# Kernel tuning notes

Measured on AMD Instinct MI355X. Metric: run time of the kernel, lower is better.

The kernel has to match this reference:

```python
import jax, jax.numpy as jnp
import numpy as np

LN2 = float(np.log(2.0))

def ssp(x):
    # ShiftedSoftplus: softplus(x) - log(2)
    return jax.nn.softplus(x) - LN2

N_NODES = 40000
N_EDGES = 640000
HIDDEN = 128
N_FILTERS = 128
N_GAUSS = 50
CUTOFF = 10.0

def setup_inputs() -> dict:
    key = jax.random.key(0)
    ks = jax.random.split(key, 12)
    s = 0.05
    x = jax.random.normal(ks[0], (N_NODES, HIDDEN), dtype=jnp.float32)
    edge_index = jax.random.randint(ks[1], (2, N_EDGES), 0, N_NODES)
    edge_weight = jax.random.uniform(ks[2], (N_EDGES,), dtype=jnp.float32) * CUTOFF
    edge_attr = jax.random.normal(ks[3], (N_EDGES, N_GAUSS), dtype=jnp.float32)
    # filter MLP params (Linear(num_gaussians,num_filters), ssp, Linear(num_filters,num_filters))
    mlp_w1 = jax.random.normal(ks[4], (N_FILTERS, N_GAUSS), dtype=jnp.float32) * s
    mlp_b1 = jnp.zeros((N_FILTERS,), dtype=jnp.float32)
    mlp_w2 = jax.random.normal(ks[5], (N_FILTERS, N_FILTERS), dtype=jnp.float32) * s
    mlp_b2 = jnp.zeros((N_FILTERS,), dtype=jnp.float32)
    # CFConv linears: lin1 (no bias), lin2 (bias)
    lin1_w = jax.random.normal(ks[6], (N_FILTERS, HIDDEN), dtype=jnp.float32) * s
    lin2_w = jax.random.normal(ks[7], (HIDDEN, N_FILTERS), dtype=jnp.float32) * s
    lin2_b = jnp.zeros((HIDDEN,), dtype=jnp.float32)
    # output linear
    lin_w = jax.random.normal(ks[8], (HIDDEN, HIDDEN), dtype=jnp.float32) * s
    lin_b = jnp.zeros((HIDDEN,), dtype=jnp.float32)
    return {
        "x": x, "edge_index": edge_index, "edge_weight": edge_weight, "edge_attr": edge_attr,
        "mlp_w1": mlp_w1, "mlp_b1": mlp_b1, "mlp_w2": mlp_w2, "mlp_b2": mlp_b2,
        "lin1_w": lin1_w, "lin2_w": lin2_w, "lin2_b": lin2_b,
        "lin_w": lin_w, "lin_b": lin_b,
    }

def reference(x, edge_index, edge_weight, edge_attr,
              mlp_w1, mlp_b1, mlp_w2, mlp_b2,
              lin1_w, lin2_w, lin2_b, lin_w, lin_b):
    src, dst = edge_index[0], edge_index[1]
    # cosine envelope
    C = 0.5 * (jnp.cos(edge_weight * jnp.pi / CUTOFF) + 1.0)  # (E,)
    # filter MLP on Gaussian-smeared distances
    W = ssp(edge_attr @ mlp_w1.T + mlp_b1) @ mlp_w2.T + mlp_b2  # (E, F)
    W = W * C[:, None]
    # CFConv: lin1 -> gather x_j -> multiply -> scatter-add -> lin2
    h = x @ lin1_w.T                                            # (N, F)
    msg = h[src] * W                                            # (E, F)
    agg = jax.ops.segment_sum(msg, dst, num_segments=x.shape[0])  # (N, F)
    h2 = agg @ lin2_w.T + lin2_b                                # (N, H)
    # activation + output projection
    out = ssp(h2) @ lin_w.T + lin_b                             # (N, H)
    return out
```

## Files before the change

### kernel.cpp

```cpp
#include <hip/hip_runtime.h>
#include <math.h>

#define LN2F 0.69314718055994531f

typedef _Float16 v8hf __attribute__((ext_vector_type(8)));
typedef float    v4f  __attribute__((ext_vector_type(4)));

__device__ __forceinline__ float ssp_fast(float x) {
    float e = __expf(-fabsf(x));
    return fmaxf(x, 0.f) + __logf(1.f + e) - LN2F;
}

__global__ __launch_bounds__(256)
void prep_kernel(const float* __restrict__ w1, const float* __restrict__ w2,
                 const float* __restrict__ l1w, const float* __restrict__ l2w,
                 const float* __restrict__ lw,
                 _Float16* __restrict__ w1f, _Float16* __restrict__ w2f,
                 _Float16* __restrict__ l1f, _Float16* __restrict__ l2f,
                 _Float16* __restrict__ lwf)
{
    int idx = blockIdx.x * 256 + threadIdx.x;
    if (idx < 8192) {
        int i = idx & 7, lane = (idx >> 3) & 63, ks = (idx >> 9) & 1, nt = idx >> 10;
        int r = nt * 16 + (lane & 15);
        int k = ks * 32 + (lane >> 4) * 8 + i;
        w1f[idx] = (k < 50) ? (_Float16)w1[r * 50 + k] : (_Float16)0.f;
        return;
    }
    int o = idx - 8192;
    if (o >= 4 * 16384) return;
    int which = o >> 14;
    int p = o & 16383;
    int i = p & 7, lane = (p >> 3) & 63, ks = (p >> 9) & 3, nt = p >> 11;
    int r = nt * 16 + (lane & 15);
    int k = ks * 32 + (lane >> 4) * 8 + i;
    const float* src = (which == 0) ? w2 : (which == 1) ? l1w : (which == 2) ? l2w : lw;
    _Float16* dst   = (which == 0) ? w2f : (which == 1) ? l1f : (which == 2) ? l2f : lwf;
    dst[p] = (_Float16)src[r * 128 + k];
}

__global__ __launch_bounds__(256)
void h_gemm_kernel(const float* __restrict__ X, const _Float16* __restrict__ Wf,
                   float* __restrict__ Y, int M)
{
    const int tid = threadIdx.x, lane = tid & 63, wv = tid >> 6;
    const int l15 = lane & 15, quad = lane >> 4;
    const int mb = blockIdx.x * 64 + wv * 16;

    const int mA = (mb + l15 < M) ? (mb + l15) : (M - 1);
    v8hf a[4];
    #pragma unroll
    for (int ks = 0; ks < 4; ++ks) {
        const float4* xp = (const float4*)&X[(size_t)mA * 128 + ks * 32 + quad * 8];
        float4 x0 = xp[0], x1 = xp[1];
        v8hf t = {(_Float16)x0.x, (_Float16)x0.y, (_Float16)x0.z, (_Float16)x0.w,
                  (_Float16)x1.x, (_Float16)x1.y, (_Float16)x1.z, (_Float16)x1.w};
        a[ks] = t;
    }
    #pragma unroll
    for (int nt = 0; nt < 8; ++nt) {
        v4f acc = {0.f, 0.f, 0.f, 0.f};
        #pragma unroll
        for (int ks = 0; ks < 4; ++ks) {
            const v8hf b = *(const v8hf*)&Wf[((nt * 4 + ks) * 64 + lane) * 8];
            acc = __builtin_amdgcn_mfma_f32_16x16x32_f16(a[ks], b, acc, 0, 0, 0);
        }
        const int col = nt * 16 + l15;
        #pragma unroll
        for (int r = 0; r < 4; ++r) {
            int row = mb + quad * 4 + r;
            if (row < M) Y[(size_t)row * 128 + col] = acc[r];
        }
    }
}

__global__ __launch_bounds__(256)
void fused_out_kernel(const float* __restrict__ agg, const _Float16* __restrict__ l2f,
                      const float* __restrict__ l2b, const _Float16* __restrict__ lwf,
                      const float* __restrict__ lb, float* __restrict__ out, int M)
{
    __shared__ __align__(16) _Float16 Sh[64 * 138];
    const int tid = threadIdx.x, lane = tid & 63, wv = tid >> 6;
    const int l15 = lane & 15, quad = lane >> 4;
    const int m0 = wv * 16;
    const int gbase = blockIdx.x * 64;

    const int mA = (gbase + m0 + l15 < M) ? (gbase + m0 + l15) : (M - 1);
    v8hf a[4];
    #pragma unroll
    for (int ks = 0; ks < 4; ++ks) {
        const float4* xp = (const float4*)&agg[(size_t)mA * 128 + ks * 32 + quad * 8];
        float4 x0 = xp[0], x1 = xp[1];
        v8hf t = {(_Float16)x0.x, (_Float16)x0.y, (_Float16)x0.z, (_Float16)x0.w,
                  (_Float16)x1.x, (_Float16)x1.y, (_Float16)x1.z, (_Float16)x1.w};
        a[ks] = t;
    }
    #pragma unroll
    for (int nt = 0; nt < 8; ++nt) {
        v4f acc = {0.f, 0.f, 0.f, 0.f};
        #pragma unroll
        for (int ks = 0; ks < 4; ++ks) {
            const v8hf b = *(const v8hf*)&l2f[((nt * 4 + ks) * 64 + lane) * 8];
            acc = __builtin_amdgcn_mfma_f32_16x16x32_f16(a[ks], b, acc, 0, 0, 0);
        }
        const float bj = l2b[nt * 16 + l15];
        #pragma unroll
        for (int r = 0; r < 4; ++r)
            Sh[(m0 + quad * 4 + r) * 138 + nt * 16 + l15] =
                (_Float16)ssp_fast(acc[r] + bj);
    }
    v8hf ua[4];
    #pragma unroll
    for (int ks = 0; ks < 4; ++ks)
        ua[ks] = *(const v8hf*)&Sh[(m0 + l15) * 138 + ks * 32 + quad * 8];

    #pragma unroll
    for (int nt = 0; nt < 8; ++nt) {
        v4f acc = {0.f, 0.f, 0.f, 0.f};
        #pragma unroll
        for (int ks = 0; ks < 4; ++ks) {
            const v8hf b = *(const v8hf*)&lwf[((nt * 4 + ks) * 64 + lane) * 8];
            acc = __builtin_amdgcn_mfma_f32_16x16x32_f16(ua[ks], b, acc, 0, 0, 0);
        }
        const int col = nt * 16 + l15;
        const float bj = lb[col];
        #pragma unroll
        for (int r = 0; r < 4; ++r) {
            int row = gbase + m0 + quad * 4 + r;
            if (row < M) out[(size_t)row * 128 + col] = acc[r] + bj;
        }
    }
}

__global__ __launch_bounds__(256, 5)
void edge_kernel(const float* __restrict__ attr,
                 const float* __restrict__ ew,
                 const int* __restrict__ srcI,
                 const int* __restrict__ dstI,
                 const _Float16* __restrict__ w1f,
                 const _Float16* __restrict__ w2f,
                 const float* __restrict__ b1,
                 const float* __restrict__ b2,
                 const float* __restrict__ h,
                 float* __restrict__ agg,
                 int E)
{
    __shared__ __align__(16) _Float16 Af[64 * 64];
    __shared__ __align__(16) _Float16 Uh[64 * 138];

    const int tid = threadIdx.x;
    const int e_base = blockIdx.x * 64;
    const int lane = tid & 63, wv = tid >> 6;
    const int m0 = wv * 16, l15 = lane & 15, quad = lane >> 4;

    float cC[4]; const float* hrow[4]; float* arow[4]; bool val[4];
    #pragma unroll
    for (int r = 0; r < 4; ++r) {
        int eg = e_base + m0 + quad * 4 + r;
        val[r] = eg < E;
        int e = val[r] ? eg : (E - 1);
        cC[r] = 0.5f * (__cosf(ew[e] * 0.31415926535897932f) + 1.f);
        hrow[r] = h + (size_t)srcI[e] * 128;
        arow[r] = agg + (size_t)dstI[e] * 128;
    }

    for (int idx = tid; idx < 4096; idx += 256) {
        int r = idx >> 6, g = idx & 63;
        int e = e_base + r;
        float v = (g < 50 && e < E) ? attr[(size_t)e * 50 + g] : 0.f;
        Af[((((r >> 4) * 2 + (g >> 5)) * 64) + (((g & 31) >> 3) * 16) + (r & 15)) * 8
           + (g & 7)] = (_Float16)v;
    }
    __syncthreads();

    float hv[8][4];
    #pragma unroll
    for (int nt = 0; nt < 8; ++nt)
        #pragma unroll
        for (int r = 0; r < 4; ++r)
            hv[nt][r] = hrow[r][nt * 16 + l15];

    const v8hf a0 = *(const v8hf*)&Af[((wv * 2 + 0) * 64 + lane) * 8];
    const v8hf a1 = *(const v8hf*)&Af[((wv * 2 + 1) * 64 + lane) * 8];
    #pragma unroll
    for (int nt = 0; nt < 8; ++nt) {
        v4f acc = {0.f, 0.f, 0.f, 0.f};
        const v8hf bA = *(const v8hf*)&w1f[((nt * 2 + 0) * 64 + lane) * 8];
        const v8hf bB = *(const v8hf*)&w1f[((nt * 2 + 1) * 64 + lane) * 8];
        acc = __builtin_amdgcn_mfma_f32_16x16x32_f16(a0, bA, acc, 0, 0, 0);
        acc = __builtin_amdgcn_mfma_f32_16x16x32_f16(a1, bB, acc, 0, 0, 0);
        const float bj = b1[nt * 16 + l15];
        #pragma unroll
        for (int r = 0; r < 4; ++r)
            Uh[(m0 + quad * 4 + r) * 138 + nt * 16 + l15] =
                (_Float16)ssp_fast(acc[r] + bj);
    }

    v8hf ua[4];
    #pragma unroll
    for (int ks = 0; ks < 4; ++ks)
        ua[ks] = *(const v8hf*)&Uh[(m0 + l15) * 138 + ks * 32 + quad * 8];

    #pragma unroll
    for (int nt = 0; nt < 8; ++nt) {
        v4f acc = {0.f, 0.f, 0.f, 0.f};
        #pragma unroll
        for (int ks = 0; ks < 4; ++ks) {
            const v8hf b = *(const v8hf*)&w2f[((nt * 4 + ks) * 64 + lane) * 8];
            acc = __builtin_amdgcn_mfma_f32_16x16x32_f16(ua[ks], b, acc, 0, 0, 0);
        }
        const int col = nt * 16 + l15;
        const float bj = b2[col];
        #pragma unroll
        for (int r = 0; r < 4; ++r) {
            if (val[r]) {
                float wf = (acc[r] + bj) * cC[r];
                atomicAdd(&arow[r][col], wf * hv[nt][r]);
            }
        }
    }
}

extern "C" void kernel_launch(void* const* d_in, const int* in_sizes, int n_in,
                              void* d_out, int out_size, void* d_ws, size_t ws_size,
                              hipStream_t stream)
{
    const float* x   = (const float*)d_in[0];
    const int*   ei  = (const int*)  d_in[1];
    const float* ew  = (const float*)d_in[2];
    const float* ea  = (const float*)d_in[3];
    const float* w1  = (const float*)d_in[4];
    const float* b1  = (const float*)d_in[5];
    const float* w2  = (const float*)d_in[6];
    const float* b2  = (const float*)d_in[7];
    const float* l1w = (const float*)d_in[8];
    const float* l2w = (const float*)d_in[9];
    const float* l2b = (const float*)d_in[10];
    const float* lw  = (const float*)d_in[11];
    const float* lb  = (const float*)d_in[12];

    const int N = in_sizes[0] / 128;
    const int E = in_sizes[2];

    float* hbuf = (float*)d_ws;
    float* agg  = hbuf + (size_t)N * 128;
    _Float16* w1f = (_Float16*)(agg + (size_t)N * 128);
    _Float16* w2f = w1f + 8192;
    _Float16* l1f = w2f + 16384;
    _Float16* l2f = l1f + 16384;
    _Float16* lwf = l2f + 16384;

    const int nb = (N + 63) / 64;

    prep_kernel<<<288, 256, 0, stream>>>(w1, w2, l1w, l2w, lw,
                                         w1f, w2f, l1f, l2f, lwf);
    hipMemsetAsync(agg, 0, (size_t)N * 128 * sizeof(float), stream);
    h_gemm_kernel<<<nb, 256, 0, stream>>>(x, l1f, hbuf, N);
    edge_kernel<<<(E + 63) / 64, 256, 0, stream>>>(ea, ew, ei, ei + E,
                                                   w1f, w2f, b1, b2, hbuf, agg, E);
    fused_out_kernel<<<nb, 256, 0, stream>>>(agg, l2f, l2b, lwf, lb, (float*)d_out, N);
}
```

Baseline: 546.4 us.

## Replace atomic scatter-add with CSR sort by destination and per-node gather

```diff
diff --git a/kernel.cpp b/kernel.cpp
--- a/kernel.cpp
+++ b/kernel.cpp
@@ -4,6 +4,7 @@
 #define LN2F 0.69314718055994531f
 
 typedef _Float16 v8hf __attribute__((ext_vector_type(8)));
+typedef _Float16 v2hf __attribute__((ext_vector_type(2)));
 typedef float    v4f  __attribute__((ext_vector_type(4)));
 
 __device__ __forceinline__ float ssp_fast(float x) {
@@ -132,6 +133,7 @@
     }
 }
 
+template<int MODE>
 __global__ __launch_bounds__(256, 5)
 void edge_kernel(const float* __restrict__ attr,
                  const float* __restrict__ ew,
@@ -143,6 +145,8 @@
                  const float* __restrict__ b2,
                  const float* __restrict__ h,
                  float* __restrict__ agg,
+                 float* __restrict__ msg32,
+                 _Float16* __restrict__ msg16,
                  int E)
 {
     __shared__ __align__(16) _Float16 Af[64 * 64];
@@ -153,15 +157,16 @@
     const int lane = tid & 63, wv = tid >> 6;
     const int m0 = wv * 16, l15 = lane & 15, quad = lane >> 4;
 
-    float cC[4]; const float* hrow[4]; float* arow[4]; bool val[4];
+    float cC[4]; const float* hrow[4]; float* arow[4]; bool val[4]; int eidx[4];
     #pragma unroll
     for (int r = 0; r < 4; ++r) {
         int eg = e_base + m0 + quad * 4 + r;
         val[r] = eg < E;
+        eidx[r] = eg;
         int e = val[r] ? eg : (E - 1);
         cC[r] = 0.5f * (__cosf(ew[e] * 0.31415926535897932f) + 1.f);
         hrow[r] = h + (size_t)srcI[e] * 128;
-        arow[r] = agg + (size_t)dstI[e] * 128;
+        if constexpr (MODE == 0) arow[r] = agg + (size_t)dstI[e] * 128;
     }
 
     for (int idx = tid; idx < 4096; idx += 256) {
@@ -214,11 +219,125 @@
         #pragma unroll
         for (int r = 0; r < 4; ++r) {
             if (val[r]) {
-                float wf = (acc[r] + bj) * cC[r];
-                atomicAdd(&arow[r][col], wf * hv[nt][r]);
+                float m = (acc[r] + bj) * cC[r] * hv[nt][r];
+                if constexpr (MODE == 0)
+                    atomicAdd(&arow[r][col], m);
+                else if constexpr (MODE == 1)
+                    msg32[(size_t)eidx[r] * 128 + col] = m;
+                else
+                    msg16[(size_t)eidx[r] * 128 + col] = (_Float16)m;
             }
         }
     }
+}
+
+__global__ __launch_bounds__(256)
+void hist_kernel(const int* __restrict__ dst, int* __restrict__ counts, int E)
+{
+    int i = blockIdx.x * 256 + threadIdx.x;
+    const int stride = gridDim.x * 256;
+    for (; i < E; i += stride) atomicAdd(&counts[dst[i]], 1);
+}
+
+__global__ __launch_bounds__(256)
+void scan1_kernel(int* __restrict__ data, int* __restrict__ bsum, int N)
+{
+    __shared__ int wsum[4];
+    const int t = threadIdx.x, lane = t & 63, wv = t >> 6;
+    const int base = blockIdx.x * 1024 + t * 4;
+    int v0 = 0, v1 = 0, v2 = 0, v3 = 0;
+    if (base + 0 < N) v0 = data[base + 0];
+    if (base + 1 < N) v1 = data[base + 1];
+    if (base + 2 < N) v2 = data[base + 2];
+    if (base + 3 < N) v3 = data[base + 3];
+    const int s = v0 + v1 + v2 + v3;
+    int sc = s;
+    #pragma unroll
+    for (int d = 1; d < 64; d <<= 1) {
+        int o = __shfl_up(sc, d);
+        if (lane >= d) sc += o;
+    }
+    if (lane == 63) wsum[wv] = sc;
+    __syncthreads();
+    int wo = 0;
+    for (int j = 0; j < wv; ++j) wo += wsum[j];
+    int run = wo + (sc - s);
+    if (base + 0 < N) data[base + 0] = run; run += v0;
+    if (base + 1 < N) data[base + 1] = run; run += v1;
+    if (base + 2 < N) data[base + 2] = run; run += v2;
+    if (base + 3 < N) data[base + 3] = run; run += v3;
+    if (t == 255) bsum[blockIdx.x] = wo + sc;
+}
+
+__global__ __launch_bounds__(256)
+void scan2_kernel(int* __restrict__ offs, const int* __restrict__ bsum,
+                  int* __restrict__ cur, int N, int E)
+{
+    int add = 0;
+    for (int j = 0; j < (int)blockIdx.x; ++j) add += bsum[j];
+    const int base = blockIdx.x * 1024 + threadIdx.x * 4;
+    #pragma unroll
+    for (int r = 0; r < 4; ++r) {
+        int i = base + r;
+        if (i < N) { int o = offs[i] + add; offs[i] = o; cur[i] = o; }
+    }
+    if (blockIdx.x == 0 && threadIdx.x == 0) offs[N] = E;
+}
+
+__global__ __launch_bounds__(256)
+void scatter_kernel(const int* __restrict__ dst, int* __restrict__ cur,
+                    int* __restrict__ perm, int E)
+{
+    int i = blockIdx.x * 256 + threadIdx.x;
+    const int stride = gridDim.x * 256;
+    for (; i < E; i += stride) {
+        int p = atomicAdd(&cur[dst[i]], 1);
+        perm[p] = i;
+    }
+}
+
+template<int MODE>
+__global__ __launch_bounds__(256)
+void gather_kernel(const float* __restrict__ msg32, const _Float16* __restrict__ msg16,
+                   const int* __restrict__ offs, const int* __restrict__ perm,
+                   float* __restrict__ agg, int N)
+{
+    const int lane = threadIdx.x & 63, wv = threadIdx.x >> 6;
+    const int n = blockIdx.x * 4 + wv;
+    if (n >= N) return;
+    const int s = offs[n], e = offs[n + 1];
+    float ax0 = 0.f, ay0 = 0.f, ax1 = 0.f, ay1 = 0.f;
+    for (int k0 = s; k0 < e; k0 += 64) {
+        const int pv = (k0 + lane < e) ? perm[k0 + lane] : 0;
+        const int cnt = min(64, e - k0);
+        int k = 0;
+        for (; k + 1 < cnt; k += 2) {
+            const int e0 = __shfl(pv, k);
+            const int e1 = __shfl(pv, k + 1);
+            if constexpr (MODE == 1) {
+                const float2 m0 = *(const float2*)&msg32[(size_t)e0 * 128 + lane * 2];
+                const float2 m1 = *(const float2*)&msg32[(size_t)e1 * 128 + lane * 2];
+                ax0 += m0.x; ay0 += m0.y; ax1 += m1.x; ay1 += m1.y;
+            } else {
+                const v2hf m0 = *(const v2hf*)&msg16[(size_t)e0 * 128 + lane * 2];
+                const v2hf m1 = *(const v2hf*)&msg16[(size_t)e1 * 128 + lane * 2];
+                ax0 += (float)m0[0]; ay0 += (float)m0[1];
+                ax1 += (float)m1[0]; ay1 += (float)m1[1];
+            }
+        }
+        if (k < cnt) {
+            const int e0 = __shfl(pv, k);
+            if constexpr (MODE == 1) {
+                const float2 m0 = *(const float2*)&msg32[(size_t)e0 * 128 + lane * 2];
+                ax0 += m0.x; ay0 += m0.y;
+            } else {
+                const v2hf m0 = *(const v2hf*)&msg16[(size_t)e0 * 128 + lane * 2];
+                ax0 += (float)m0[0]; ay0 += (float)m0[1];
+            }
+        }
+    }
+    float2 o; o.x = ax0 + ax1; o.y = ay0 + ay1;
+    *(float2*)&agg[(size_t)n * 128 + lane * 2] = o;
 }
 
 extern "C" void kernel_launch(void* const* d_in, const int* in_sizes, int n_in,
@@ -241,22 +360,64 @@
 
     const int N = in_sizes[0] / 128;
     const int E = in_sizes[2];
-
-    float* hbuf = (float*)d_ws;
-    float* agg  = hbuf + (size_t)N * 128;
-    _Float16* w1f = (_Float16*)(agg + (size_t)N * 128);
-    _Float16* w2f = w1f + 8192;
-    _Float16* l1f = w2f + 16384;
-    _Float16* l2f = l1f + 16384;
-    _Float16* lwf = l2f + 16384;
+    const int NB = (N + 1023) / 1024;
+
+    char* base = (char*)d_ws;
+    size_t off = 0;
+    auto take = [&](size_t bytes) -> char* {
+        char* r = base + off;
+        off = (off + bytes + 255) & ~(size_t)255;
+        return r;
+    };
+    float*    hbuf = (float*)   take((size_t)N * 128 * 4);
+    float*    agg  = (float*)   take((size_t)N * 128 * 4);
+    _Float16* w1f  = (_Float16*)take(8192 * 2);
+    _Float16* w2f  = (_Float16*)take(16384 * 2);
+    _Float16* l1f  = (_Float16*)take(16384 * 2);
+    _Float16* l2f  = (_Float16*)take(16384 * 2);
+    _Float16* lwf  = (_Float16*)take(16384 * 2);
+    int*      offs = (int*)     take((size_t)(N + 1) * 4);
+    int*      cur  = (int*)     take((size_t)N * 4);
+    int*      bsum = (int*)     take((size_t)NB * 4);
+    int*      perm = (int*)     take((size_t)E * 4);
+    const size_t base_bytes = off;
+
+    int mode;
+    if      (ws_size >= base_bytes + (size_t)E * 128 * 4) mode = 1;
+    else if (ws_size >= base_bytes + (size_t)E * 128 * 2) mode = 2;
+    else                                                  mode = 0;
+    float*    msg32 = (float*)   (base + off);
+    _Float16* msg16 = (_Float16*)(base + off);
 
     const int nb = (N + 63) / 64;
+    const int eb = (E + 63) / 64;
+    const int tb = (E + 255) / 256;
 
     prep_kernel<<<288, 256, 0, stream>>>(w1, w2, l1w, l2w, lw,
                                          w1f, w2f, l1f, l2f, lwf);
-    hipMemsetAsync(agg, 0, (size_t)N * 128 * sizeof(float), stream);
     h_gemm_kernel<<<nb, 256, 0, stream>>>(x, l1f, hbuf, N);
-    edge_kernel<<<(E + 63) / 64, 256, 0, stream>>>(ea, ew, ei, ei + E,
-                                                   w1f, w2f, b1, b2, hbuf, agg, E);
+
+    if (mode == 0) {
+        hipMemsetAsync(agg, 0, (size_t)N * 128 * sizeof(float), stream);
+        edge_kernel<0><<<eb, 256, 0, stream>>>(ea, ew, ei, ei + E, w1f, w2f, b1, b2,
+                                               hbuf, agg, nullptr, nullptr, E);
+    } else {
+        hipMemsetAsync(offs, 0, (size_t)(N + 1) * sizeof(int), stream);
+        hist_kernel<<<tb, 256, 0, stream>>>(ei + E, offs, E);
+        scan1_kernel<<<NB, 256, 0, stream>>>(offs, bsum, N);
+        scan2_kernel<<<NB, 256, 0, stream>>>(offs, bsum, cur, N, E);
+        scatter_kernel<<<tb, 256, 0, stream>>>(ei + E, cur, perm, E);
+        if (mode == 1) {
+            edge_kernel<1><<<eb, 256, 0, stream>>>(ea, ew, ei, ei + E, w1f, w2f, b1, b2,
+                                                   hbuf, nullptr, msg32, nullptr, E);
+            gather_kernel<1><<<(N + 3) / 4, 256, 0, stream>>>(msg32, nullptr, offs, perm,
+                                                              agg, N);
+        } else {
+            edge_kernel<2><<<eb, 256, 0, stream>>>(ea, ew, ei, ei + E, w1f, w2f, b1, b2,
+                                                   hbuf, nullptr, nullptr, msg16, E);
+            gather_kernel<2><<<(N + 3) / 4, 256, 0, stream>>>(nullptr, msg16, offs, perm,
+                                                              agg, N);
+        }
+    }
     fused_out_kernel<<<nb, 256, 0, stream>>>(agg, l2f, l2b, lwf, lb, (float*)d_out, N);
 }
```

Result: slower. 606.7 us (+11.0%).
